# Kernel tuning notes

Hardware: AMD Instinct MI355X
Metric: run time of the kernel (lower is better)

## Reference

```python
import jax, jax.numpy as jnp
import numpy as np

NR = 5000            # number of sampled center points
H, W = 480, 640      # depth map resolution
P = NR * (NR - 1) // 2  # number of ordered pairs (i < j) = 12,497,500


def setup_inputs() -> dict:
    key = jax.random.key(0)
    k1, k2, k3, k4 = jax.random.split(key, 4)
    x = jax.random.normal(k1, (H, W), dtype=jnp.float32)
    rows = jax.random.randint(k2, (NR,), 0, H)
    cols = jax.random.randint(k3, (NR,), 0, W)
    centers = jnp.stack([rows, cols], axis=1).astype(jnp.int32)  # [NR, 2]
    # relative-depth ground truth labels in {-1, 0, +1}; mask = |gt|
    gt = jax.random.randint(k4, (P,), -1, 2).astype(jnp.float32)
    return {"x": x, "gt": gt, "centers": centers}


def reference(x, gt, centers):
    # gather predicted depths at the NR sampled pixel locations
    z = x[centers[:, 0], centers[:, 1]]            # [NR]
    # all pairs i<j in the same row-major order as the original double loop
    ii, jj = jnp.triu_indices(NR, k=1)             # each [P]
    d = z[ii] - z[jj]                              # z_A - z_B, [P]
    mask = jnp.abs(gt)                             # [P]
    # logistic ranking loss where gt != 0, squared loss where gt == 0
    loss = mask * jnp.log1p(jnp.exp(-gt * d)) + (1.0 - mask) * d * d
    return jnp.sum(loss) / jnp.float32(P)
```

## Files before the change

kernel.cpp:

```cpp
#include <hip/hip_runtime.h>
#include <stdint.h>

#define NR 5000
#define NRM1 4999
#define W 640
#define NBLK 2500
#define NG 5
#define PCOUNT 12497500.0f
#define LOG2E 1.44269504088896340736f
#define LN2   0.69314718055994530942f

typedef float f32x2  __attribute__((ext_vector_type(2)));
typedef float float4u __attribute__((ext_vector_type(4)));
struct __attribute__((packed, aligned(4))) f4wrap { float4u v; };
__device__ __forceinline__ float4u load4u(const float* p) {
    return ((const f4wrap*)p)->v;
}

__global__ void gather_z(const float* __restrict__ x,
                         const int* __restrict__ centers,
                         float* __restrict__ z) {
    int t = blockIdx.x * blockDim.x + threadIdx.x;
    if (t < NR) {
        const int2 rc = ((const int2*)centers)[t];
        z[t] = x[rc.x * W + rc.y];
    }
}

__global__ __launch_bounds__(256) void pair_loss(const float* __restrict__ gt,
                                                 const float* __restrict__ z,
                                                 float* __restrict__ partials) {
    __shared__ float sz[NR];
    __shared__ float wsum[4];
    const int tid = threadIdx.x;
    const int b = blockIdx.x;

    const float4* __restrict__ zf4 = (const float4*)z;
    for (int t = tid; t < NR / 4; t += 256)
        *(float4*)&sz[4 * t] = zf4[t];
    __syncthreads();

    const int r1 = b, r2 = NR - 2 - b;
    const int len1 = NRM1 - r1;
    const int off1 = r1 * NRM1 - (r1 * (r1 - 1)) / 2;
    const int off2 = r2 * NRM1 - (r2 * (r2 - 1)) / 2;
    const int off2v = off2 - len1;
    const int vmax = (r2 > r1) ? 5000 : len1;
    const float zr1 = sz[r1], zr2 = sz[r2];

    float4u g4[NG];
    int cb[NG];
    #pragma unroll
    for (int k = 0; k < NG; ++k) {
        const int vb = 4 * tid + 1024 * k;
        const int c = min(vb, vmax - 4);
        cb[k] = c;
        const float* base = (c < len1) ? (gt + off1) : (gt + off2v);
        g4[k] = load4u(base + c);
    }

    f32x2 acc0 = {0.0f, 0.0f}, acc1 = {0.0f, 0.0f};
    float accS = 0.0f;

    #pragma unroll
    for (int k = 0; k < NG; ++k) {
        const int c = cb[k];
        const int vb = 4 * tid + 1024 * k;
        const bool in1 = c < len1;
        const bool straddle = in1 && (c + 3 >= len1);
        if (!straddle) {
            const float zr = in1 ? zr1 : zr2;
            const int ib = c + (in1 ? r1 + 1 : 0);
            const f32x2 zj0 = { sz[ib],     sz[ib + 1] };
            const f32x2 zj1 = { sz[ib + 2], sz[ib + 3] };
            const f32x2 gg0 = { g4[k].x, g4[k].y };
            const f32x2 gg1 = { g4[k].z, g4[k].w };
            const f32x2 s0 = zj0 - zr,  s1 = zj1 - zr;
            const f32x2 sl0 = s0 * LOG2E, sl1 = s1 * LOG2E;
            const f32x2 t0 = gg0 * sl0, t1 = gg1 * sl1;
            const f32x2 e0 = { exp2f(t0.x), exp2f(t0.y) };
            const f32x2 e1 = { exp2f(t1.x), exp2f(t1.y) };
            const f32x2 p0 = e0 + 1.0f, p1 = e1 + 1.0f;
            const f32x2 lg0 = { __log2f(p0.x), __log2f(p0.y) };
            const f32x2 lg1 = { __log2f(p1.x), __log2f(p1.y) };
            const f32x2 q0 = s0 * sl0, q1 = s1 * sl1;
            const f32x2 m0 = gg0 * gg0, m1 = gg1 * gg1;
            const f32x2 l0 = q0 + m0 * (lg0 - q0);
            const f32x2 l1 = q1 + m1 * (lg1 - q1);
            const float w = (vb < vmax) ? 1.0f : 0.0f;
            acc0 += l0 * w;
            acc1 += l1 * w;
        } else if (vb < vmax) {
            #pragma unroll
            for (int e = 0; e < 4; ++e) {
                const int ce = c + e;
                const bool i1 = ce < len1;
                const float zj = sz[ce + (i1 ? r1 + 1 : 0)];
                const float zr = i1 ? zr1 : zr2;
                const float g = gt[(i1 ? off1 : off2v) + ce];
                const float s  = zj - zr;
                const float sl = s * LOG2E;
                const float lg = __log2f(1.0f + exp2f(g * sl));
                accS += (g != 0.0f) ? lg : s * sl;
            }
        }
    }

    const f32x2 accp = acc0 + acc1;
    float acc = accp.x + accp.y + accS;

    for (int o = 32; o > 0; o >>= 1) acc += __shfl_down(acc, o, 64);
    if ((tid & 63) == 0) wsum[tid >> 6] = acc;
    __syncthreads();
    if (tid == 0)
        partials[b] = (wsum[0] + wsum[1]) + (wsum[2] + wsum[3]);
}

__global__ __launch_bounds__(256) void final_reduce(const float* __restrict__ partials,
                                                    float* __restrict__ out) {
    __shared__ float wsum[4];
    float acc = 0.0f;
    const float4* __restrict__ p4 = (const float4*)partials;
    for (int t = threadIdx.x; t < NBLK / 4; t += 256) {
        const float4 v = p4[t];
        acc += (v.x + v.y) + (v.z + v.w);
    }
    for (int o = 32; o > 0; o >>= 1) acc += __shfl_down(acc, o, 64);
    if ((threadIdx.x & 63) == 0) wsum[threadIdx.x >> 6] = acc;
    __syncthreads();
    if (threadIdx.x == 0)
        out[0] = ((wsum[0] + wsum[1]) + (wsum[2] + wsum[3])) * (LN2 / PCOUNT);
}

extern "C" void kernel_launch(void* const* d_in, const int* in_sizes, int n_in,
                              void* d_out, int out_size, void* d_ws, size_t ws_size,
                              hipStream_t stream) {
    const float* x       = (const float*)d_in[0];
    const float* gt      = (const float*)d_in[1];
    const int*   centers = (const int*)d_in[2];
    float* out = (float*)d_out;

    float* z        = (float*)d_ws;
    float* partials = z + NR;

    gather_z<<<(NR + 255) / 256, 256, 0, stream>>>(x, centers, z);
    pair_loss<<<NBLK, 256, 0, stream>>>(gt, z, partials);
    final_reduce<<<1, 256, 0, stream>>>(partials, out);
}
```

Measured before the change: 25.61 us.

## Compute pairwise ranking loss in packed fp16 with prescaled half-precision depths

Stores gathered depths as fp16 pre-multiplied by log2(e), and keeps two shared-memory copies (aligned and shifted by one) so any pair of consecutive depths loads as one half2. The main loop then does the subtraction, exp2, log2 and accumulation with packed half2 instructions instead of fp32. The goal is to halve VALU and transcendental cost in the pair loop. In exchange the loss is computed in fp16, with less accurate exp/log and half-precision per-thread accumulation, which risks tolerance failures.

Result: slower. 27.58 us (+7.7%).

```diff
diff --git a/kernel.cpp b/kernel.cpp
--- a/kernel.cpp
+++ b/kernel.cpp
@@ -1,4 +1,5 @@
 #include <hip/hip_runtime.h>
+#include <hip/hip_fp16.h>
 #include <stdint.h>
 
 #define NR 5000
@@ -10,7 +11,6 @@
 #define LOG2E 1.44269504088896340736f
 #define LN2   0.69314718055994530942f
 
-typedef float f32x2  __attribute__((ext_vector_type(2)));
 typedef float float4u __attribute__((ext_vector_type(4)));
 struct __attribute__((packed, aligned(4))) f4wrap { float4u v; };
 __device__ __forceinline__ float4u load4u(const float* p) {
@@ -19,26 +19,35 @@
 
 __global__ void gather_z(const float* __restrict__ x,
                          const int* __restrict__ centers,
-                         float* __restrict__ z) {
+                         __half* __restrict__ zs) {
     int t = blockIdx.x * blockDim.x + threadIdx.x;
     if (t < NR) {
         const int2 rc = ((const int2*)centers)[t];
-        z[t] = x[rc.x * W + rc.y];
+        zs[t] = __float2half(x[rc.x * W + rc.y] * LOG2E);
+    } else if (t < NR + 2) {
+        zs[t] = __float2half(0.0f);
     }
 }
 
 __global__ __launch_bounds__(256) void pair_loss(const float* __restrict__ gt,
-                                                 const float* __restrict__ z,
+                                                 const __half* __restrict__ zs,
                                                  float* __restrict__ partials) {
-    __shared__ float sz[NR];
+    __shared__ __half2 A2[NR / 2 + 2];
+    __shared__ __half2 B2[NR / 2 + 2];
     __shared__ float wsum[4];
     const int tid = threadIdx.x;
     const int b = blockIdx.x;
 
-    const float4* __restrict__ zf4 = (const float4*)z;
-    for (int t = tid; t < NR / 4; t += 256)
-        *(float4*)&sz[4 * t] = zf4[t];
+    const __half2* __restrict__ zs2 = (const __half2*)zs;
+    for (int t = tid; t < NR / 2; t += 256) {
+        const __half2 a  = zs2[t];
+        const __half2 an = zs2[t + 1];
+        A2[t] = a;
+        B2[t] = __halves2half2(__high2half(a), __low2half(an));
+    }
     __syncthreads();
+
+    const __half* __restrict__ szh = (const __half*)A2;
 
     const int r1 = b, r2 = NR - 2 - b;
     const int len1 = NRM1 - r1;
@@ -46,7 +55,9 @@
     const int off2 = r2 * NRM1 - (r2 * (r2 - 1)) / 2;
     const int off2v = off2 - len1;
     const int vmax = (r2 > r1) ? 5000 : len1;
-    const float zr1 = sz[r1], zr2 = sz[r2];
+    const __half zr1h = szh[r1], zr2h = szh[r2];
+    const __half2 zr1h2 = __half2half2(zr1h), zr2h2 = __half2half2(zr2h);
+    const float zr1f = __half2float(zr1h), zr2f = __half2float(zr2h);
 
     float4u g4[NG];
     int cb[NG];
@@ -59,7 +70,10 @@
         g4[k] = load4u(base + c);
     }
 
-    f32x2 acc0 = {0.0f, 0.0f}, acc1 = {0.0f, 0.0f};
+    const __half2 one2  = __float2half2_rn(1.0f);
+    const __half2 zero2 = __float2half2_rn(0.0f);
+    const __half2 ln2h2 = __float2half2_rn(LN2);
+    __half2 accA = zero2, accB = zero2;
     float accS = 0.0f;
 
     #pragma unroll
@@ -69,45 +83,45 @@
         const bool in1 = c < len1;
         const bool straddle = in1 && (c + 3 >= len1);
         if (!straddle) {
-            const float zr = in1 ? zr1 : zr2;
             const int ib = c + (in1 ? r1 + 1 : 0);
-            const f32x2 zj0 = { sz[ib],     sz[ib + 1] };
-            const f32x2 zj1 = { sz[ib + 2], sz[ib + 3] };
-            const f32x2 gg0 = { g4[k].x, g4[k].y };
-            const f32x2 gg1 = { g4[k].z, g4[k].w };
-            const f32x2 s0 = zj0 - zr,  s1 = zj1 - zr;
-            const f32x2 sl0 = s0 * LOG2E, sl1 = s1 * LOG2E;
-            const f32x2 t0 = gg0 * sl0, t1 = gg1 * sl1;
-            const f32x2 e0 = { exp2f(t0.x), exp2f(t0.y) };
-            const f32x2 e1 = { exp2f(t1.x), exp2f(t1.y) };
-            const f32x2 p0 = e0 + 1.0f, p1 = e1 + 1.0f;
-            const f32x2 lg0 = { __log2f(p0.x), __log2f(p0.y) };
-            const f32x2 lg1 = { __log2f(p1.x), __log2f(p1.y) };
-            const f32x2 q0 = s0 * sl0, q1 = s1 * sl1;
-            const f32x2 m0 = gg0 * gg0, m1 = gg1 * gg1;
-            const f32x2 l0 = q0 + m0 * (lg0 - q0);
-            const f32x2 l1 = q1 + m1 * (lg1 - q1);
-            const float w = (vb < vmax) ? 1.0f : 0.0f;
-            acc0 += l0 * w;
-            acc1 += l1 * w;
+            const __half2* __restrict__ arr = (ib & 1) ? B2 : A2;
+            const int i0 = ib >> 1;
+            const __half2 zj01 = arr[i0];
+            const __half2 zj23 = arr[i0 + 1];
+            const __half2 zrh2 = in1 ? zr1h2 : zr2h2;
+            const __half2 g01 = __float22half2_rn(make_float2(g4[k].x, g4[k].y));
+            const __half2 g23 = __float22half2_rn(make_float2(g4[k].z, g4[k].w));
+            const __half2 s01 = __hsub2(zj01, zrh2), s23 = __hsub2(zj23, zrh2);
+            const __half2 t01 = __hmul2(g01, s01),  t23 = __hmul2(g23, s23);
+            const __half2 p01 = __hadd2(h2exp2(t01), one2);
+            const __half2 p23 = __hadd2(h2exp2(t23), one2);
+            const __half2 lg01 = h2log2(p01), lg23 = h2log2(p23);
+            const __half2 q01 = __hmul2(__hmul2(s01, s01), ln2h2);
+            const __half2 q23 = __hmul2(__hmul2(s23, s23), ln2h2);
+            const __half2 m01 = __hmul2(g01, g01), m23 = __hmul2(g23, g23);
+            const __half2 l01 = __hfma2(m01, __hsub2(lg01, q01), q01);
+            const __half2 l23 = __hfma2(m23, __hsub2(lg23, q23), q23);
+            const __half2 w2 = (vb < vmax) ? one2 : zero2;
+            accA = __hfma2(l01, w2, accA);
+            accB = __hfma2(l23, w2, accB);
         } else if (vb < vmax) {
             #pragma unroll
             for (int e = 0; e < 4; ++e) {
                 const int ce = c + e;
                 const bool i1 = ce < len1;
-                const float zj = sz[ce + (i1 ? r1 + 1 : 0)];
-                const float zr = i1 ? zr1 : zr2;
+                const float zj = __half2float(szh[ce + (i1 ? r1 + 1 : 0)]);
+                const float zr = i1 ? zr1f : zr2f;
                 const float g = gt[(i1 ? off1 : off2v) + ce];
-                const float s  = zj - zr;
-                const float sl = s * LOG2E;
-                const float lg = __log2f(1.0f + exp2f(g * sl));
-                accS += (g != 0.0f) ? lg : s * sl;
+                const float s = zj - zr;
+                const float lg = __log2f(1.0f + exp2f(g * s));
+                accS += (g != 0.0f) ? lg : s * s * LN2;
             }
         }
     }
 
-    const f32x2 accp = acc0 + acc1;
-    float acc = accp.x + accp.y + accS;
+    const float2 fA = __half22float2(accA);
+    const float2 fB = __half22float2(accB);
+    float acc = ((fA.x + fA.y) + (fB.x + fB.y)) + accS;
 
     for (int o = 32; o > 0; o >>= 1) acc += __shfl_down(acc, o, 64);
     if ((tid & 63) == 0) wsum[tid >> 6] = acc;
@@ -140,10 +154,10 @@
     const int*   centers = (const int*)d_in[2];
     float* out = (float*)d_out;
 
-    float* z        = (float*)d_ws;
-    float* partials = z + NR;
+    float* partials = (float*)d_ws;
+    __half* zs      = (__half*)(partials + NBLK);
 
-    gather_z<<<(NR + 255) / 256, 256, 0, stream>>>(x, centers, z);
-    pair_loss<<<NBLK, 256, 0, stream>>>(gt, z, partials);
+    gather_z<<<(NR + 2 + 255) / 256, 256, 0, stream>>>(x, centers, zs);
+    pair_loss<<<NBLK, 256, 0, stream>>>(gt, zs, partials);
     final_reduce<<<1, 256, 0, stream>>>(partials, out);
 }
```
